# Kernel optimization log

Measured on AMD Instinct MI355X. Metric: run time of the kernel, lower is better.

## Reference

```python
import jax, jax.numpy as jnp
import numpy as np

B, N, D = 32, 2048, 320

def _init(key, shape, fan_in):
    return jax.random.normal(key, shape, dtype=jnp.float32) / np.sqrt(fan_in).astype(np.float32)

def setup_inputs() -> dict:
    key = jax.random.key(0)
    ks = jax.random.split(key, 11)
    return {
        "x": jax.random.normal(ks[0], (B, N, D), dtype=jnp.float32),
        # downs MLP: 320->160->80
        "W1": _init(ks[1], (320, 160), 320), "b1": jnp.zeros((160,), jnp.float32),
        "W2": _init(ks[2], (160, 80), 160),  "b2": jnp.zeros((80,), jnp.float32),
        # GraphConv1d layers: 80->40, 40->5
        "Wg1": _init(ks[3], (80, 40), 80),   "bg1": jnp.zeros((40,), jnp.float32),
        "Wg2": _init(ks[4], (40, 5), 40),    "bg2": jnp.zeros((5,), jnp.float32),
        # final classifier: 5->2
        "Wf": _init(ks[5], (5, 2), 5),       "bf": jnp.zeros((2,), jnp.float32),
    }

def _euclidean_adj(h):
    # h: [B, N, C] -> row-softmax of negative squared pairwise Euclidean distance [B, N, N]
    sq = jnp.sum(h * h, axis=-1, keepdims=True)               # [B, N, 1]
    d2 = sq - 2.0 * jnp.einsum('bnc,bmc->bnm', h, h) + jnp.swapaxes(sq, -1, -2)
    return jax.nn.softmax(-d2, axis=-1)

def _graph_conv(h, W, b):
    a = _euclidean_adj(h)                                     # dynamic adjacency
    agg = jnp.einsum('bnm,bmc->bnc', a, h)                    # neighbor aggregation
    return jax.nn.relu(agg @ W + b)

def reference(x, W1, b1, W2, b2, Wg1, bg1, Wg2, bg2, Wf, bf):
    h = jax.nn.relu(x @ W1 + b1)          # [B, N, 160]
    h = jax.nn.relu(h @ W2 + b2)          # [B, N, 80]
    h = _graph_conv(h, Wg1, bg1)          # [B, N, 40]
    h = _graph_conv(h, Wg2, bg2)          # [B, N, 5]
    h = jnp.mean(h, axis=1)               # Mean() over nodes -> [B, 5]
    logits = h @ Wf + bf                  # [B, 2]
    return jax.nn.softmax(logits, axis=-1)
```

## Files before the change

### kernel.cpp

```cpp
#include <hip/hip_runtime.h>
#include <math.h>

#define BB 32
#define NN 2048
#define D_IN 320
#define H1 160
#define H2 80
#define H4 5

typedef __attribute__((ext_vector_type(8))) short short8;
typedef __attribute__((ext_vector_type(4))) short short4v;
typedef __attribute__((ext_vector_type(4))) float f32x4;
typedef __attribute__((ext_vector_type(16))) float f32x16;

__device__ inline ushort f2bf(float f) {
    union { float f; unsigned u; } v; v.f = f;
    unsigned r = v.u + 0x7fff + ((v.u >> 16) & 1);
    return (ushort)(r >> 16);
}
__device__ inline float bf2f(ushort u) {
    union { float f; unsigned u; } v; v.u = ((unsigned)u) << 16;
    return v.f;
}
__device__ inline unsigned pkbf(float hi, float lo) {
    union { float f; unsigned u; } a, b; a.f = hi; b.f = lo;
    return __builtin_amdgcn_perm(a.u + 0x8000u, b.u + 0x8000u, 0x07060302u);
}
__device__ inline float fexp2(float x) {
    float r;
    asm("v_exp_f32 %0, %1" : "=v"(r) : "v"(x));
    return r;
}
union U2S { unsigned u[2]; short4v s; };
union U4S { unsigned u[4]; short8 s; short4v h[2]; };

#define LOG2E  1.44269504088896340736f
#define TWOL2E 2.88539008177792681472f

__global__ __launch_bounds__(256) void prep_weights_kernel(
    const float* __restrict__ W1, const float* __restrict__ W2,
    const float* __restrict__ Wg1, const float* __restrict__ bg1,
    const float* __restrict__ Wg2, const float* __restrict__ bg2,
    ushort* __restrict__ Wt1, ushort* __restrict__ Wt2,
    ushort* __restrict__ Wg1B, float* __restrict__ bg1P,
    ushort* __restrict__ Wg2A, float* __restrict__ bg2P)
{
    const int id0 = blockIdx.x * 256 + threadIdx.x;
    const int stride = gridDim.x * 256;
    for (int i = id0; i < H1 * D_IN; i += stride) {
        const int j = i / D_IN, c = i % D_IN;
        Wt1[i] = f2bf(W1[c * H1 + j]);
    }
    for (int i = id0; i < H2 * H1; i += stride) {
        const int j = i / H1, c = i % H1;
        Wt2[i] = f2bf(W2[c * H2 + j]);
    }
    for (int i = id0; i < 48 * 96; i += stride) {
        const int j = i / 96, c = i % 96;
        Wg1B[i] = (j < 40 && c < 80) ? f2bf(Wg1[c * 40 + j]) : (ushort)0;
    }
    for (int i = id0; i < 32 * 48; i += stride) {
        const int j = i / 48, c = i % 48;
        const int c4 = c & 15;
        const int pos = (c & ~15) + (c4 & 3) + (((c4 >> 3) & 1) << 2) + (((c4 >> 2) & 1) << 3);
        Wg2A[j * 48 + pos] = (j < 5 && c < 40) ? f2bf(Wg2[c * 5 + j]) : (ushort)0;
    }
    if (id0 < 64) bg1P[id0] = (id0 < 40) ? bg1[id0] : 0.f;
    if (id0 < 32) bg2P[id0] = (id0 < 5) ? bg2[id0] : 0.f;
}

__global__ __launch_bounds__(256) void mlp_mfma_kernel(
    const float* __restrict__ x,
    const ushort* __restrict__ Wt1, const float* __restrict__ b1,
    const ushort* __restrict__ Wt2, const float* __restrict__ b2,
    const ushort* __restrict__ Wg1B,
    ushort* __restrict__ h2, ushort* __restrict__ V1T, float* __restrict__ sq2)
{
    constexpr int XST  = 72;
    constexpr int W1ST = 72;
    constexpr int H1ST = 168;
    constexpr int RST  = 104;

    __shared__ __attribute__((aligned(16))) ushort h1t[64 * H1ST];
    __shared__ __attribute__((aligned(16))) ushort ws1[H1 * W1ST];
    __shared__ float b1s[H1];
    __shared__ float b2s[H2];

    ushort* xs = h1t;

    const int t = threadIdx.x;
    const int lane = t & 63, w = t >> 6;
    const int colid = lane & 15, quad = lane >> 4;
    const int i = blockIdx.x;
    const int b = ((i & 7) << 2) + ((i >> 3) & 3);
    const int n0 = (i >> 5) * 64;
    const int row0 = b * NN + n0;

    if (t < H1) b1s[t] = b1[t];
    if (t < H2) b2s[t] = b2[t];

    f32x4 c1[10];
    #pragma unroll
    for (int ns = 0; ns < 10; ++ns) c1[ns] = (f32x4){0.f, 0.f, 0.f, 0.f};

    float4 xr[4];
    short8 wr[5];
    {
        #pragma unroll
        for (int i2 = 0; i2 < 4; ++i2) {
            const int id = t + i2 * 256, row = id >> 4, c4 = id & 15;
            xr[i2] = *(const float4*)&x[(size_t)(row0 + row) * D_IN + c4 * 4];
        }
        #pragma unroll
        for (int i2 = 0; i2 < 5; ++i2) {
            const int id = t + i2 * 256, j = id >> 3, part = id & 7;
            wr[i2] = *(const short8*)&Wt1[j * D_IN + part * 8];
        }
    }

    for (int kc = 0; kc < 5; ++kc) {
        if (kc) __syncthreads();
        #pragma unroll
        for (int i2 = 0; i2 < 4; ++i2) {
            const int id = t + i2 * 256, row = id >> 4, c4 = id & 15;
            uint2 up;
            up.x = pkbf(xr[i2].y, xr[i2].x);
            up.y = pkbf(xr[i2].w, xr[i2].z);
            *(uint2*)&xs[row * XST + c4 * 4] = up;
        }
        #pragma unroll
        for (int i2 = 0; i2 < 5; ++i2) {
            const int id = t + i2 * 256, j = id >> 3, part = id & 7;
            *(short8*)&ws1[j * W1ST + part * 8] = wr[i2];
        }
        __syncthreads();
        if (kc < 4) {
            const int k0 = (kc + 1) * 64;
            #pragma unroll
            for (int i2 = 0; i2 < 4; ++i2) {
                const int id = t + i2 * 256, row = id >> 4, c4 = id & 15;
                xr[i2] = *(const float4*)&x[(size_t)(row0 + row) * D_IN + k0 + c4 * 4];
            }
            #pragma unroll
            for (int i2 = 0; i2 < 5; ++i2) {
                const int id = t + i2 * 256, j = id >> 3, part = id & 7;
                wr[i2] = *(const short8*)&Wt1[j * D_IN + k0 + part * 8];
            }
        }

        short8 af[2];
        #pragma unroll
        for (int kf = 0; kf < 2; ++kf)
            af[kf] = *(const short8*)&xs[(w * 16 + colid) * XST + kf * 32 + quad * 8];
        #pragma unroll
        for (int ns = 0; ns < 10; ++ns) {
            #pragma unroll
            for (int kf = 0; kf < 2; ++kf) {
                const short8 bf = *(const short8*)&ws1[(ns * 16 + colid) * W1ST + kf * 32 + quad * 8];
                c1[ns] = __builtin_amdgcn_mfma_f32_16x16x32_bf16(af[kf], bf, c1[ns], 0, 0, 0);
            }
        }
    }
    __syncthreads();

    #pragma unroll
    for (int ns = 0; ns < 10; ++ns) {
        const float bj = b1s[ns * 16 + colid];
        #pragma unroll
        for (int r = 0; r < 4; ++r)
            h1t[(w * 16 + quad * 4 + r) * H1ST + ns * 16 + colid] =
                f2bf(fmaxf(c1[ns][r] + bj, 0.f));
    }
    __asm__ volatile("s_waitcnt lgkmcnt(0)" ::: "memory");

    short8 a2[5];
    #pragma unroll
    for (int kf = 0; kf < 5; ++kf)
        a2[kf] = *(const short8*)&h1t[(w * 16 + colid) * H1ST + kf * 32 + quad * 8];

    f32x4 c2[5];
    #pragma unroll
    for (int js = 0; js < 5; ++js) {
        f32x4 acc = (f32x4){0.f, 0.f, 0.f, 0.f};
        #pragma unroll
        for (int kf = 0; kf < 5; ++kf) {
            const short8 wb = *(const short8*)&Wt2[(js * 16 + colid) * H1 + kf * 32 + quad * 8];
            acc = __builtin_amdgcn_mfma_f32_16x16x32_bf16(a2[kf], wb, acc, 0, 0, 0);
        }
        c2[js] = acc;
    }
    __syncthreads();

    ushort* h2row = h1t;
    float rsq[4] = {0.f, 0.f, 0.f, 0.f};
    #pragma unroll
    for (int js = 0; js < 5; ++js) {
        const float bj = b2s[js * 16 + colid];
        #pragma unroll
        for (int r = 0; r < 4; ++r) {
            const ushort u = f2bf(fmaxf(c2[js][r] + bj, 0.f));
            const float vv = bf2f(u);
            rsq[r] += vv * vv;
            h2[(size_t)(row0 + w * 16 + quad * 4 + r) * 80 + js * 16 + colid] = u;
            h2row[(w * 16 + quad * 4 + r) * RST + js * 16 + colid] = u;
        }
    }
    {
        const int zr = t >> 2, zc = t & 3;
        *(short4v*)&h2row[zr * RST + 80 + zc * 4] = (short4v){0, 0, 0, 0};
    }
    __asm__ volatile("s_waitcnt lgkmcnt(0)" ::: "memory");

    short8 a3[3];
    #pragma unroll
    for (int kf = 0; kf < 3; ++kf)
        a3[kf] = *(const short8*)&h2row[(w * 16 + colid) * RST + kf * 32 + quad * 8];

    f32x4 c3[3];
    #pragma unroll
    for (int js = 0; js < 3; ++js) {
        f32x4 acc = (f32x4){0.f, 0.f, 0.f, 0.f};
        #pragma unroll
        for (int kf = 0; kf < 3; ++kf) {
            const short8 wb = *(const short8*)&Wg1B[(js * 16 + colid) * 96 + kf * 32 + quad * 8];
            acc = __builtin_amdgcn_mfma_f32_16x16x32_bf16(a3[kf], wb, acc, 0, 0, 0);
        }
        c3[js] = acc;
    }

    #pragma unroll
    for (int m = 1; m <= 8; m <<= 1)
        #pragma unroll
        for (int r = 0; r < 4; ++r) rsq[r] += __shfl_xor(rsq[r], m);
    if (colid == 0) {
        #pragma unroll
        for (int r = 0; r < 4; ++r)
            sq2[(size_t)row0 + w * 16 + quad * 4 + r] = rsq[r] * 0.5f;
    }

    ushort* Tbuf = ws1;
    #pragma unroll
    for (int js = 0; js < 3; ++js)
        #pragma unroll
        for (int r = 0; r < 4; ++r)
            Tbuf[(js * 16 + colid) * 72 + w * 16 + quad * 4 + r] = f2bf(c3[js][r]);
    __syncthreads();
    const short8 ones8 = {16256, 16256, 16256, 16256, 16256, 16256, 16256, 16256};
    for (int id = t; id < 48 * 8; id += 256) {
        const int row = id >> 3, part = id & 7;
        const short8 val = (row == 40) ? ones8 : *(const short8*)&Tbuf[row * 72 + part * 8];
        *(short8*)&V1T[((size_t)b * 48 + row) * NN + n0 + part * 8] = val;
    }
}

template<int CK, int CV, int CVS, int ONES_CH, bool HAS_OUT, bool DO_MEAN, int C_OUT>
__global__ __launch_bounds__(512, 2) void attn_conv_kernel(
    const ushort* __restrict__ h, const ushort* __restrict__ hT,
    const float* __restrict__ sqg,
    const ushort* __restrict__ WtP, const float* __restrict__ biasP,
    ushort* __restrict__ ho, ushort* __restrict__ hoT, float* __restrict__ sqo,
    float* __restrict__ mean_out)
{
    constexpr int CF   = CK / 16;
    constexpr int CSV  = CV / 32;
    constexpr int KST  = CK + 8;
    constexpr int VST  = 64 + 8;
    constexpr int KPR  = CK / 8;
    constexpr int KTOT = 64 * KPR;
    constexpr int NK   = (KTOT + 255) / 256;
    constexpr int VTOT = CVS * 8;
    constexpr int NV   = (VTOT + 255) / 256;
    constexpr int TST  = 136;
    constexpr int CS1  = ONES_CH / 32;
    constexpr int R1v  = ((ONES_CH % 32) / 8) * 4 + (ONES_CH & 3);
    constexpr int BUFN = 64 * KST + CVS * VST;
    constexpr int NITH = NN / 128;
    constexpr int ESTR = CSV * 16 + 4;

    __shared__ __attribute__((aligned(16))) ushort ldsbuf[2][2][BUFN];
    __shared__ __attribute__((aligned(16))) float sqs[2][2][64];

    const int t = threadIdx.x;
    const int lane = t & 63, w = t >> 6;
    const int qw = w & 3, kh = w >> 2;
    const int th = t & 255;
    const int m32 = lane & 31, hl = lane >> 5;
    const int i = blockIdx.x;
    const int b = ((i & 7) << 2) + ((i >> 3) & 3);
    const int n0blk = (i >> 5) * 128;
    const int qrow = n0blk + qw * 32 + m32;
    const int kbase = kh * (NN / 2);

    short8 qf[CF];
    {
        const ushort* qr = h + ((size_t)b * NN + qrow) * CK;
        #pragma unroll
        for (int c = 0; c < CF; ++c)
            qf[c] = *(const short8*)&qr[c * 16 + hl * 8];
    }
    const float nsqn = -sqg[(size_t)b * NN + qrow];

    f32x16 o[CSV];
    #pragma unroll
    for (int cs = 0; cs < CSV; ++cs)
        #pragma unroll
        for (int r = 0; r < 16; ++r) o[cs][r] = 0.f;

    short8 kreg[NK], vreg[NV];
    float sqreg = 0.f;

    auto loadTile = [&](int n1) {
        const ushort* hsrc = h + ((size_t)b * NN + n1) * CK;
        #pragma unroll
        for (int i2 = 0; i2 < NK; ++i2) {
            const int id = th + i2 * 256;
            if (KTOT % 256 == 0 || id < KTOT)
                kreg[i2] = *(const short8*)&hsrc[id * 8];
        }
        #pragma unroll
        for (int i2 = 0; i2 < NV; ++i2) {
            const int id = th + i2 * 256;
            if (VTOT % 256 == 0 || id < VTOT) {
                const int c = id >> 3, pt = id & 7;
                vreg[i2] = *(const short8*)&hT[((size_t)b * CVS + c) * NN + n1 + pt * 8];
            }
        }
        if (th < 64) sqreg = sqg[(size_t)b * NN + n1 + th];
    };
    auto stageTile = [&](int buf) {
        ushort* Kd = ldsbuf[kh][buf];
        ushort* Vd = Kd + 64 * KST;
        #pragma unroll
        for (int i2 = 0; i2 < NK; ++i2) {
            const int id = th + i2 * 256;
            if (KTOT % 256 == 0 || id < KTOT) {
                const int row = id / KPR, pt = id % KPR;
                *(short8*)&Kd[row * KST + pt * 8] = kreg[i2];
            }
        }
        #pragma unroll
        for (int i2 = 0; i2 < NV; ++i2) {
            const int id = th + i2 * 256;
            if (VTOT % 256 == 0 || id < VTOT) {
                const int c = id >> 3, pt = id & 7;
                const int colb = ((pt >> 1) << 4) + ((pt & 1) << 2);
                U4S vv; vv.s = vreg[i2];
                *(short4v*)&Vd[c * VST + colb]     = vv.h[0];
                *(short4v*)&Vd[c * VST + colb + 8] = vv.h[1];
            }
        }
        if (th < 64) sqs[kh][buf][th] = sqreg;
    };

    auto preloadK = [&](const ushort* Krow, short8 (&kf)[2][CF]) {
        #pragma unroll
        for (int T = 0; T < 2; ++T)
            #pragma unroll
            for (int c = 0; c < CF; ++c)
                kf[T][c] = *(const short8*)&Krow[(T * 32 + m32) * KST + c * 16 + hl * 8];
    };
    auto initST = [&](int buf, f32x16& s0, f32x16& s1) {
        #pragma unroll
        for (int g = 0; g < 4; ++g) {
            const f32x4 sm0 = *(const f32x4*)&sqs[kh][buf][g * 8 + hl * 4];
            const f32x4 sm1 = *(const f32x4*)&sqs[kh][buf][32 + g * 8 + hl * 4];
            #pragma unroll
            for (int r2 = 0; r2 < 4; ++r2) {
                s0[g * 4 + r2] = nsqn - sm0[r2];
                s1[g * 4 + r2] = nsqn - sm1[r2];
            }
        }
    };
    auto smfma = [&](short8 (&kf)[2][CF], f32x16& s0, f32x16& s1) {
        #pragma unroll
        for (int c = 0; c < CF; ++c) {
            s0 = __builtin_amdgcn_mfma_f32_32x32x16_bf16(kf[0][c], qf[c], s0, 0, 0, 0);
            s1 = __builtin_amdgcn_mfma_f32_32x32x16_bf16(kf[1][c], qf[c], s1, 0, 0, 0);
        }
    };
    auto readV = [&](const ushort* Vcol, short8 (&vf)[2][2][CSV]) {
        const short8 z8 = {0, 0, 0, 0, 0, 0, 0, 0};
        #pragma unroll
        for (int T = 0; T < 2; ++T)
            #pragma unroll
            for (int c = 0; c < 2; ++c)
                #pragma unroll
                for (int cs = 0; cs < CSV; ++cs) {
                    const int row = cs * 32 + m32;
                    vf[T][c][cs] = (row < CVS)
                        ? *(const short8*)&Vcol[row * VST + (T * 2 + c) * 16 + hl * 8]
                        : z8;
                }
    };
    auto expPV = [&](const f32x16& s0, const f32x16& s1, const short8 (&vf)[2][2][CSV]) {
        #pragma unroll
        for (int T = 0; T < 2; ++T) {
            const f32x16& st = T ? s1 : s0;
            float p[16];
            #pragma unroll
            for (int g = 0; g < 4; ++g)
                #pragma unroll
                for (int r2 = 0; r2 < 4; ++r2)
                    p[g * 4 + r2] = fexp2(st[g * 4 + r2] * TWOL2E);
            #pragma unroll
            for (int c = 0; c < 2; ++c) {
                U4S pk_;
                #pragma unroll
                for (int bq = 0; bq < 4; ++bq)
                    pk_.u[bq] = pkbf(p[c * 8 + bq * 2 + 1], p[c * 8 + bq * 2]);
                #pragma unroll
                for (int cs = 0; cs < CSV; ++cs)
                    o[cs] = __builtin_amdgcn_mfma_f32_32x32x16_bf16(vf[T][c][cs], pk_.s, o[cs], 0, 0, 0);
            }
        }
    };

    loadTile(kbase);
    stageTile(0);
    __syncthreads();
    loadTile(kbase + 64);

    #pragma unroll 1
    for (int it = 0; it < NITH; ++it) {
        const int cur = it & 1;
        const ushort* Krow = ldsbuf[kh][cur];
        const ushort* Vcol = Krow + 64 * KST;

        short8 kf[2][CF];
        f32x16 s0, s1;
        preloadK(Krow, kf);
        initST(cur, s0, s1);

        if (it + 1 < NITH) stageTile(cur ^ 1);
        if (it + 2 < NITH) loadTile(kbase + (it + 2) * 64);

        smfma(kf, s0, s1);
        short8 vf[2][2][CSV];
        readV(Vcol, vf);
        expPV(s0, s1, vf);
        __syncthreads();
    }

    float* exch = (float*)&ldsbuf[0][0][0];
    if (kh == 1) {
        #pragma unroll
        for (int cs = 0; cs < CSV; ++cs)
            #pragma unroll
            for (int g = 0; g < 4; ++g) {
                f32x4 v;
                #pragma unroll
                for (int j = 0; j < 4; ++j) v[j] = o[cs][g * 4 + j];
                *(f32x4*)&exch[(qw * 64 + lane) * ESTR + cs * 16 + g * 4] = v;
            }
    }
    __syncthreads();
    if (kh == 0) {
        #pragma unroll
        for (int cs = 0; cs < CSV; ++cs)
            #pragma unroll
            for (int g = 0; g < 4; ++g) {
                const f32x4 v = *(const f32x4*)&exch[(qw * 64 + lane) * ESTR + cs * 16 + g * 4];
                #pragma unroll
                for (int j = 0; j < 4; ++j) o[cs][g * 4 + j] += v[j];
            }
    }

    float rsv = (hl == 0) ? o[CS1][R1v] : 0.f;
    rsv += __shfl_xor(rsv, 32);
    const float rinv = 1.f / rsv;

    if constexpr (DO_MEAN) {
        if (kh == 0) {
            float msum[4];
            #pragma unroll
            for (int r2 = 0; r2 < 4; ++r2)
                msum[r2] = fmaxf(o[0][r2] * rinv + biasP[hl * 4 + r2], 0.f);
            #pragma unroll
            for (int s = 1; s <= 16; s <<= 1)
                #pragma unroll
                for (int r2 = 0; r2 < 4; ++r2) msum[r2] += __shfl_xor(msum[r2], s);
            if (m32 == 0) {
                if (hl == 0) {
                    #pragma unroll
                    for (int r2 = 0; r2 < 4; ++r2)
                        atomicAdd(&mean_out[b * C_OUT + r2], msum[r2] * (1.f / NN));
                } else {
                    atomicAdd(&mean_out[b * C_OUT + 4], msum[0] * (1.f / NN));
                }
            }
        }
    }

    if constexpr (HAS_OUT) {
        __syncthreads();
        ushort* Tbuf = (ushort*)&ldsbuf[0][0][0];
        if (kh == 0) {
            float vv[CSV][16];
            float rsq = 0.f;
            #pragma unroll
            for (int cs = 0; cs < CSV; ++cs) {
                #pragma unroll
                for (int g = 0; g < 4; ++g) {
                    const int jb = cs * 32 + g * 8 + hl * 4;
                    const f32x4 bv = *(const f32x4*)&biasP[jb];
                    float v[4];
                    #pragma unroll
                    for (int r2 = 0; r2 < 4; ++r2) {
                        float val = fmaxf(o[cs][g * 4 + r2] * rinv + bv[r2], 0.f);
                        if (cs == CS1 && g * 4 + r2 == R1v) val = 0.f;
                        v[r2] = val;
                        vv[cs][g * 4 + r2] = val;
                    }
                    if (jb < 48) {
                        U2S uo;
                        uo.u[0] = pkbf(v[1], v[0]);
                        uo.u[1] = pkbf(v[3], v[2]);
                        *(short4v*)&ho[((size_t)b * NN + qrow) * 48 + jb] = uo.s;
                        #pragma unroll
                        for (int r2 = 0; r2 < 4; ++r2) {
                            const float vs = bf2f((ushort)(uo.u[r2 >> 1] >> ((r2 & 1) * 16)));
                            rsq += vs * vs;
                        }
                    }
                }
            }
            const float rsq2 = rsq + __shfl_xor(rsq, 32);
            if (hl == 0) sqo[(size_t)b * NN + qrow] = rsq2 * 0.5f;

            short8 ob2[3];
            #pragma unroll
            for (int cc = 0; cc < 3; ++cc) {
                const int cs = cc >> 1, c2 = cc & 1;
                U4S ob_;
                #pragma unroll
                for (int bq = 0; bq < 4; ++bq)
                    ob_.u[bq] = pkbf(vv[cs][c2 * 8 + bq * 2 + 1], vv[cs][c2 * 8 + bq * 2]);
                ob2[cc] = ob_.s;
            }
            f32x16 acc;
            #pragma unroll
            for (int r = 0; r < 16; ++r) acc[r] = 0.f;
            #pragma unroll
            for (int cc = 0; cc < 3; ++cc) {
                const short8 wa = *(const short8*)&WtP[(size_t)m32 * 48 + cc * 16 + hl * 8];
                acc = __builtin_amdgcn_mfma_f32_32x32x16_bf16(wa, ob2[cc], acc, 0, 0, 0);
            }

            #pragma unroll
            for (int g = 0; g < 2; ++g)
                #pragma unroll
                for (int r2 = 0; r2 < 4; ++r2)
                    Tbuf[(g * 8 + hl * 4 + r2) * TST + qw * 32 + m32] = f2bf(acc[g * 4 + r2]);
        }
        __syncthreads();
        const short8 ones8 = {16256, 16256, 16256, 16256, 16256, 16256, 16256, 16256};
        if (t < 256) {
            const int row = t >> 4, part = t & 15;
            const short8 val = (row == 8) ? ones8
                             : *(const short8*)&Tbuf[row * TST + part * 8];
            *(short8*)&hoT[((size_t)b * 16 + row) * NN + n0blk + part * 8] = val;
        }
    }
}

__global__ __launch_bounds__(64) void final_kernel(
    const float* __restrict__ mean, const float* __restrict__ Wf,
    const float* __restrict__ bf, float* __restrict__ out)
{
    const int t = threadIdx.x;
    const int b = t >> 1, k = t & 1;
    float acc = bf[k];
    #pragma unroll
    for (int c = 0; c < H4; ++c) acc += mean[b * H4 + c] * Wf[c * 2 + k];
    const float other = __shfl_xor(acc, 1);
    const float mx = fmaxf(acc, other);
    const float e  = __expf(acc - mx);
    const float eo = __expf(other - mx);
    out[t] = e / (e + eo);
}

extern "C" void kernel_launch(void* const* d_in, const int* in_sizes, int n_in,
                              void* d_out, int out_size, void* d_ws, size_t ws_size,
                              hipStream_t stream) {
    const float* x   = (const float*)d_in[0];
    const float* W1  = (const float*)d_in[1];
    const float* b1  = (const float*)d_in[2];
    const float* W2  = (const float*)d_in[3];
    const float* b2  = (const float*)d_in[4];
    const float* Wg1 = (const float*)d_in[5];
    const float* bg1 = (const float*)d_in[6];
    const float* Wg2 = (const float*)d_in[7];
    const float* bg2 = (const float*)d_in[8];
    const float* Wf  = (const float*)d_in[9];
    const float* bf  = (const float*)d_in[10];

    ushort* h2   = (ushort*)d_ws;
    ushort* V1T  = h2  + (size_t)BB * NN * 80;
    float*  sq2  = (float*)(V1T + (size_t)BB * 48 * NN);
    ushort* h3   = (ushort*)(sq2 + (size_t)BB * NN);
    ushort* V2T  = h3  + (size_t)BB * NN * 48;
    float*  sq3  = (float*)(V2T + (size_t)BB * 16 * NN);
    float*  meanb = sq3 + (size_t)BB * NN;
    ushort* Wt1  = (ushort*)(meanb + 160);
    ushort* Wt2  = Wt1 + (size_t)H1 * D_IN;
    ushort* Wg1B = Wt2 + (size_t)H2 * H1;
    float*  bg1P = (float*)(Wg1B + 48 * 96);
    ushort* Wg2A = (ushort*)(bg1P + 64);
    float*  bg2P = (float*)(Wg2A + 32 * 48);

    hipMemsetAsync(meanb, 0, BB * H4 * sizeof(float), stream);

    prep_weights_kernel<<<64, 256, 0, stream>>>(W1, W2, Wg1, bg1, Wg2, bg2,
                                                Wt1, Wt2, Wg1B, bg1P, Wg2A, bg2P);
    mlp_mfma_kernel<<<BB * NN / 64, 256, 0, stream>>>(x, Wt1, b1, Wt2, b2, Wg1B,
                                                      h2, V1T, sq2);
    attn_conv_kernel<80, 64, 48, 40, true,  false, 0><<<BB * NN / 128, 512, 0, stream>>>(
        h2, V1T, sq2, Wg2A, bg1P, h3, V2T, sq3, nullptr);
    attn_conv_kernel<48, 32, 16, 8,  false, true,  5><<<BB * NN / 128, 512, 0, stream>>>(
        h3, V2T, sq3, nullptr, bg2P, nullptr, nullptr, nullptr, meanb);
    final_kernel<<<1, 64, 0, stream>>>(meanb, Wf, bf, (float*)d_out);
}
```

Before: 273.0 us.

## Split attention-conv into separate key-split partial and combine kernels

The fused 512-thread attention kernel, which split keys across two wave halves and reduced them through LDS, is replaced by a 256-thread partial kernel launched per key-split block, plus a combine kernel. The partial kernel writes fp32 partial accumulators to global memory, and the combine kernel sums them and applies the normalization, bias, ReLU, next-layer projection and mean epilogue. The aim is finer-grained blocks for better scheduling and occupancy, and a shorter epilogue. The cost is extra launches and a global round trip for the partial outputs.

```diff
diff --git a/kernel.cpp b/kernel.cpp
--- a/kernel.cpp
+++ b/kernel.cpp
@@ -253,13 +253,10 @@
     }
 }
 
-template<int CK, int CV, int CVS, int ONES_CH, bool HAS_OUT, bool DO_MEAN, int C_OUT>
-__global__ __launch_bounds__(512, 2) void attn_conv_kernel(
+template<int CK, int CV, int CVS, int KSPLIT>
+__global__ __launch_bounds__(256, 2) void attn_part_kernel(
     const ushort* __restrict__ h, const ushort* __restrict__ hT,
-    const float* __restrict__ sqg,
-    const ushort* __restrict__ WtP, const float* __restrict__ biasP,
-    ushort* __restrict__ ho, ushort* __restrict__ hoT, float* __restrict__ sqo,
-    float* __restrict__ mean_out)
+    const float* __restrict__ sqg, float* __restrict__ pO)
 {
     constexpr int CF   = CK / 16;
     constexpr int CSV  = CV / 32;
@@ -270,26 +267,22 @@
     constexpr int NK   = (KTOT + 255) / 256;
     constexpr int VTOT = CVS * 8;
     constexpr int NV   = (VTOT + 255) / 256;
-    constexpr int TST  = 136;
-    constexpr int CS1  = ONES_CH / 32;
-    constexpr int R1v  = ((ONES_CH % 32) / 8) * 4 + (ONES_CH & 3);
     constexpr int BUFN = 64 * KST + CVS * VST;
-    constexpr int NITH = NN / 128;
-    constexpr int ESTR = CSV * 16 + 4;
-
-    __shared__ __attribute__((aligned(16))) ushort ldsbuf[2][2][BUFN];
-    __shared__ __attribute__((aligned(16))) float sqs[2][2][64];
+    constexpr int NITH = NN / 64 / KSPLIT;
+
+    __shared__ __attribute__((aligned(16))) ushort ldsbuf[2][BUFN];
+    __shared__ __attribute__((aligned(16))) float sqs[2][64];
 
     const int t = threadIdx.x;
     const int lane = t & 63, w = t >> 6;
-    const int qw = w & 3, kh = w >> 2;
-    const int th = t & 255;
     const int m32 = lane & 31, hl = lane >> 5;
-    const int i = blockIdx.x;
-    const int b = ((i & 7) << 2) + ((i >> 3) & 3);
-    const int n0blk = (i >> 5) * 128;
-    const int qrow = n0blk + qw * 32 + m32;
-    const int kbase = kh * (NN / 2);
+    const int gi = blockIdx.x;
+    const int ks = gi & (KSPLIT - 1);
+    const int qblk = gi / KSPLIT;
+    const int b = ((qblk & 7) << 2) + ((qblk >> 3) & 3);
+    const int n0blk = (qblk >> 5) * 128;
+    const int qrow = n0blk + w * 32 + m32;
+    const int kbase = ks * (NN / KSPLIT);
 
     short8 qf[CF];
     {
@@ -313,26 +306,26 @@
         const ushort* hsrc = h + ((size_t)b * NN + n1) * CK;
         #pragma unroll
         for (int i2 = 0; i2 < NK; ++i2) {
-            const int id = th + i2 * 256;
+            const int id = t + i2 * 256;
             if (KTOT % 256 == 0 || id < KTOT)
                 kreg[i2] = *(const short8*)&hsrc[id * 8];
         }
         #pragma unroll
         for (int i2 = 0; i2 < NV; ++i2) {
-            const int id = th + i2 * 256;
+            const int id = t + i2 * 256;
             if (VTOT % 256 == 0 || id < VTOT) {
                 const int c = id >> 3, pt = id & 7;
                 vreg[i2] = *(const short8*)&hT[((size_t)b * CVS + c) * NN + n1 + pt * 8];
             }
         }
-        if (th < 64) sqreg = sqg[(size_t)b * NN + n1 + th];
+        if (t < 64) sqreg = sqg[(size_t)b * NN + n1 + t];
     };
     auto stageTile = [&](int buf) {
-        ushort* Kd = ldsbuf[kh][buf];
+        ushort* Kd = ldsbuf[buf];
         ushort* Vd = Kd + 64 * KST;
         #pragma unroll
         for (int i2 = 0; i2 < NK; ++i2) {
-            const int id = th + i2 * 256;
+            const int id = t + i2 * 256;
             if (KTOT % 256 == 0 || id < KTOT) {
                 const int row = id / KPR, pt = id % KPR;
                 *(short8*)&Kd[row * KST + pt * 8] = kreg[i2];
@@ -340,7 +333,7 @@
         }
         #pragma unroll
         for (int i2 = 0; i2 < NV; ++i2) {
-            const int id = th + i2 * 256;
+            const int id = t + i2 * 256;
             if (VTOT % 256 == 0 || id < VTOT) {
                 const int c = id >> 3, pt = id & 7;
                 const int colb = ((pt >> 1) << 4) + ((pt & 1) << 2);
@@ -349,7 +342,7 @@
                 *(short4v*)&Vd[c * VST + colb + 8] = vv.h[1];
             }
         }
-        if (th < 64) sqs[kh][buf][th] = sqreg;
+        if (t < 64) sqs[buf][t] = sqreg;
     };
 
     auto preloadK = [&](const ushort* Krow, short8 (&kf)[2][CF]) {
@@ -362,8 +355,8 @@
     auto initST = [&](int buf, f32x16& s0, f32x16& s1) {
         #pragma unroll
         for (int g = 0; g < 4; ++g) {
-            const f32x4 sm0 = *(const f32x4*)&sqs[kh][buf][g * 8 + hl * 4];
-            const f32x4 sm1 = *(const f32x4*)&sqs[kh][buf][32 + g * 8 + hl * 4];
+            const f32x4 sm0 = *(const f32x4*)&sqs[buf][g * 8 + hl * 4];
+            const f32x4 sm1 = *(const f32x4*)&sqs[buf][32 + g * 8 + hl * 4];
             #pragma unroll
             for (int r2 = 0; r2 < 4; ++r2) {
                 s0[g * 4 + r2] = nsqn - sm0[r2];
@@ -423,7 +416,7 @@
     #pragma unroll 1
     for (int it = 0; it < NITH; ++it) {
         const int cur = it & 1;
-        const ushort* Krow = ldsbuf[kh][cur];
+        const ushort* Krow = ldsbuf[cur];
         const ushort* Vcol = Krow + 64 * KST;
 
         short8 kf[2][CF];
@@ -441,120 +434,132 @@
         __syncthreads();
     }
 
-    float* exch = (float*)&ldsbuf[0][0][0];
-    if (kh == 1) {
+    #pragma unroll
+    for (int cs = 0; cs < CSV; ++cs)
+        #pragma unroll
+        for (int r = 0; r < 16; ++r)
+            pO[((((size_t)qblk * KSPLIT + ks) * CSV + cs) * 16 + r) * 256 + t] = o[cs][r];
+}
+
+template<int CV, int CVS, int ONES_CH, bool HAS_OUT, bool DO_MEAN, int C_OUT, int KSPLIT>
+__global__ __launch_bounds__(256) void attn_combine_kernel(
+    const float* __restrict__ pO,
+    const ushort* __restrict__ WtP, const float* __restrict__ biasP,
+    ushort* __restrict__ ho, ushort* __restrict__ hoT, float* __restrict__ sqo,
+    float* __restrict__ mean_out)
+{
+    constexpr int CSV = CV / 32;
+    constexpr int TST = 136;
+    constexpr int CS1 = ONES_CH / 32;
+    constexpr int R1v = ((ONES_CH % 32) / 8) * 4 + (ONES_CH & 3);
+
+    __shared__ __attribute__((aligned(16))) ushort Tbuf[16 * TST];
+
+    const int t = threadIdx.x;
+    const int lane = t & 63, w = t >> 6;
+    const int m32 = lane & 31, hl = lane >> 5;
+    const int i = blockIdx.x;
+    const int b = ((i & 7) << 2) + ((i >> 3) & 3);
+    const int n0blk = (i >> 5) * 128;
+    const int qrow = n0blk + w * 32 + m32;
+
+    f32x16 o[CSV];
+    #pragma unroll
+    for (int cs = 0; cs < CSV; ++cs)
+        #pragma unroll
+        for (int r = 0; r < 16; ++r) o[cs][r] = 0.f;
+    #pragma unroll
+    for (int ks = 0; ks < KSPLIT; ++ks)
         #pragma unroll
         for (int cs = 0; cs < CSV; ++cs)
             #pragma unroll
-            for (int g = 0; g < 4; ++g) {
-                f32x4 v;
-                #pragma unroll
-                for (int j = 0; j < 4; ++j) v[j] = o[cs][g * 4 + j];
-                *(f32x4*)&exch[(qw * 64 + lane) * ESTR + cs * 16 + g * 4] = v;
-            }
-    }
-    __syncthreads();
-    if (kh == 0) {
-        #pragma unroll
-        for (int cs = 0; cs < CSV; ++cs)
-            #pragma unroll
-            for (int g = 0; g < 4; ++g) {
-                const f32x4 v = *(const f32x4*)&exch[(qw * 64 + lane) * ESTR + cs * 16 + g * 4];
-                #pragma unroll
-                for (int j = 0; j < 4; ++j) o[cs][g * 4 + j] += v[j];
-            }
-    }
+            for (int r = 0; r < 16; ++r)
+                o[cs][r] += pO[((((size_t)i * KSPLIT + ks) * CSV + cs) * 16 + r) * 256 + t];
 
     float rsv = (hl == 0) ? o[CS1][R1v] : 0.f;
     rsv += __shfl_xor(rsv, 32);
     const float rinv = 1.f / rsv;
 
     if constexpr (DO_MEAN) {
-        if (kh == 0) {
-            float msum[4];
-            #pragma unroll
-            for (int r2 = 0; r2 < 4; ++r2)
-                msum[r2] = fmaxf(o[0][r2] * rinv + biasP[hl * 4 + r2], 0.f);
-            #pragma unroll
-            for (int s = 1; s <= 16; s <<= 1)
+        float msum[4];
+        #pragma unroll
+        for (int r2 = 0; r2 < 4; ++r2)
+            msum[r2] = fmaxf(o[0][r2] * rinv + biasP[hl * 4 + r2], 0.f);
+        #pragma unroll
+        for (int s = 1; s <= 16; s <<= 1)
+            #pragma unroll
+            for (int r2 = 0; r2 < 4; ++r2) msum[r2] += __shfl_xor(msum[r2], s);
+        if (m32 == 0) {
+            if (hl == 0) {
                 #pragma unroll
-                for (int r2 = 0; r2 < 4; ++r2) msum[r2] += __shfl_xor(msum[r2], s);
-            if (m32 == 0) {
-                if (hl == 0) {
-                    #pragma unroll
-                    for (int r2 = 0; r2 < 4; ++r2)
-                        atomicAdd(&mean_out[b * C_OUT + r2], msum[r2] * (1.f / NN));
-                } else {
-                    atomicAdd(&mean_out[b * C_OUT + 4], msum[0] * (1.f / NN));
+                for (int r2 = 0; r2 < 4; ++r2)
+                    atomicAdd(&mean_out[b * C_OUT + r2], msum[r2] * (1.f / NN));
+            } else {
+                atomicAdd(&mean_out[b * C_OUT + 4], msum[0] * (1.f / NN));
+            }
+        }
+    }
+
+    if constexpr (HAS_OUT) {
+        float vv[CSV][16];
+        float rsq = 0.f;
+        #pragma unroll
+        for (int cs = 0; cs < CSV; ++cs) {
+            #pragma unroll
+            for (int g = 0; g < 4; ++g) {
+                const int jb = cs * 32 + g * 8 + hl * 4;
+                const f32x4 bv = *(const f32x4*)&biasP[jb];
+                float v[4];
+                #pragma unroll
+                for (int r2 = 0; r2 < 4; ++r2) {
+                    float val = fmaxf(o[cs][g * 4 + r2] * rinv + bv[r2], 0.f);
+                    if (cs == CS1 && g * 4 + r2 == R1v) val = 0.f;
+                    v[r2] = val;
+                    vv[cs][g * 4 + r2] = val;
                 }
-            }
-        }
-    }
-
-    if constexpr (HAS_OUT) {
-        __syncthreads();
-        ushort* Tbuf = (ushort*)&ldsbuf[0][0][0];
-        if (kh == 0) {
-            float vv[CSV][16];
-            float rsq = 0.f;
-            #pragma unroll
-            for (int cs = 0; cs < CSV; ++cs) {
-                #pragma unroll
-                for (int g = 0; g < 4; ++g) {
-                    const int jb = cs * 32 + g * 8 + hl * 4;
-                    const f32x4 bv = *(const f32x4*)&biasP[jb];
-                    float v[4];
+                if (jb < 48) {
+                    U2S uo;
+                    uo.u[0] = pkbf(v[1], v[0]);
+                    uo.u[1] = pkbf(v[3], v[2]);
+                    *(short4v*)&ho[((size_t)b * NN + qrow) * 48 + jb] = uo.s;
                     #pragma unroll
                     for (int r2 = 0; r2 < 4; ++r2) {
-                        float val = fmaxf(o[cs][g * 4 + r2] * rinv + bv[r2], 0.f);
-                        if (cs == CS1 && g * 4 + r2 == R1v) val = 0.f;
-                        v[r2] = val;
-                        vv[cs][g * 4 + r2] = val;
-                    }
-                    if (jb < 48) {
-                        U2S uo;
-                        uo.u[0] = pkbf(v[1], v[0]);
-                        uo.u[1] = pkbf(v[3], v[2]);
-                        *(short4v*)&ho[((size_t)b * NN + qrow) * 48 + jb] = uo.s;
-                        #pragma unroll
-                        for (int r2 = 0; r2 < 4; ++r2) {
-                            const float vs = bf2f((ushort)(uo.u[r2 >> 1] >> ((r2 & 1) * 16)));
-                            rsq += vs * vs;
-                        }
+                        const float vs = bf2f((ushort)(uo.u[r2 >> 1] >> ((r2 & 1) * 16)));
+                        rsq += vs * vs;
                     }
                 }
             }
-            const float rsq2 = rsq + __shfl_xor(rsq, 32);
-            if (hl == 0) sqo[(size_t)b * NN + qrow] = rsq2 * 0.5f;
-
-            short8 ob2[3];
-            #pragma unroll
-            for (int cc = 0; cc < 3; ++cc) {
-                const int cs = cc >> 1, c2 = cc & 1;
-                U4S ob_;
-                #pragma unroll
-                for (int bq = 0; bq < 4; ++bq)
-                    ob_.u[bq] = pkbf(vv[cs][c2 * 8 + bq * 2 + 1], vv[cs][c2 * 8 + bq * 2]);
-                ob2[cc] = ob_.s;
-            }
-            f32x16 acc;
-            #pragma unroll
-            for (int r = 0; r < 16; ++r) acc[r] = 0.f;
-            #pragma unroll
-            for (int cc = 0; cc < 3; ++cc) {
-                const short8 wa = *(const short8*)&WtP[(size_t)m32 * 48 + cc * 16 + hl * 8];
-                acc = __builtin_amdgcn_mfma_f32_32x32x16_bf16(wa, ob2[cc], acc, 0, 0, 0);
-            }
-
-            #pragma unroll
-            for (int g = 0; g < 2; ++g)
-                #pragma unroll
-                for (int r2 = 0; r2 < 4; ++r2)
-                    Tbuf[(g * 8 + hl * 4 + r2) * TST + qw * 32 + m32] = f2bf(acc[g * 4 + r2]);
-        }
+        }
+        const float rsq2 = rsq + __shfl_xor(rsq, 32);
+        if (hl == 0) sqo[(size_t)b * NN + qrow] = rsq2 * 0.5f;
+
+        short8 ob2[3];
+        #pragma unroll
+        for (int cc = 0; cc < 3; ++cc) {
+            const int cs = cc >> 1, c2 = cc & 1;
+            U4S ob_;
+            #pragma unroll
+            for (int bq = 0; bq < 4; ++bq)
+                ob_.u[bq] = pkbf(vv[cs][c2 * 8 + bq * 2 + 1], vv[cs][c2 * 8 + bq * 2]);
+            ob2[cc] = ob_.s;
+        }
+        f32x16 acc;
+        #pragma unroll
+        for (int r = 0; r < 16; ++r) acc[r] = 0.f;
+        #pragma unroll
+        for (int cc = 0; cc < 3; ++cc) {
+            const short8 wa = *(const short8*)&WtP[(size_t)m32 * 48 + cc * 16 + hl * 8];
+            acc = __builtin_amdgcn_mfma_f32_32x32x16_bf16(wa, ob2[cc], acc, 0, 0, 0);
+        }
+
+        #pragma unroll
+        for (int g = 0; g < 2; ++g)
+            #pragma unroll
+            for (int r2 = 0; r2 < 4; ++r2)
+                Tbuf[(g * 8 + hl * 4 + r2) * TST + w * 32 + m32] = f2bf(acc[g * 4 + r2]);
         __syncthreads();
         const short8 ones8 = {16256, 16256, 16256, 16256, 16256, 16256, 16256, 16256};
-        if (t < 256) {
+        {
             const int row = t >> 4, part = t & 15;
             const short8 val = (row == 8) ? ones8
                              : *(const short8*)&Tbuf[row * TST + part * 8];
@@ -607,6 +612,7 @@
     float*  bg1P = (float*)(Wg1B + 48 * 96);
     ushort* Wg2A = (ushort*)(bg1P + 64);
     float*  bg2P = (float*)(Wg2A + 32 * 48);
+    float*  pO   = bg2P + 32;
 
     hipMemsetAsync(meanb, 0, BB * H4 * sizeof(float), stream);
 
@@ -614,9 +620,13 @@
                                                 Wt1, Wt2, Wg1B, bg1P, Wg2A, bg2P);
     mlp_mfma_kernel<<<BB * NN / 64, 256, 0, stream>>>(x, Wt1, b1, Wt2, b2, Wg1B,
                                                       h2, V1T, sq2);
-    attn_conv_kernel<80, 64, 48, 40, true,  false, 0><<<BB * NN / 128, 512, 0, stream>>>(
-        h2, V1T, sq2, Wg2A, bg1P, h3, V2T, sq3, nullptr);
-    attn_conv_kernel<48, 32, 16, 8,  false, true,  5><<<BB * NN / 128, 512, 0, stream>>>(
-        h3, V2T, sq3, nullptr, bg2P, nullptr, nullptr, nullptr, meanb);
+    attn_part_kernel<80, 64, 48, 2><<<BB * NN / 128 * 2, 256, 0, stream>>>(
+        h2, V1T, sq2, pO);
+    attn_combine_kernel<64, 48, 40, true, false, 0, 2><<<BB * NN / 128, 256, 0, stream>>>(
+        pO, Wg2A, bg1P, h3, V2T, sq3, nullptr);
+    attn_part_kernel<48, 32, 16, 2><<<BB * NN / 128 * 2, 256, 0, stream>>>(
+        h3, V2T, sq3, pO);
+    attn_combine_kernel<32, 16, 8, false, true, 5, 2><<<BB * NN / 128, 256, 0, stream>>>(
+        pO, nullptr, bg2P, nullptr, nullptr, nullptr, meanb);
     final_kernel<<<1, 64, 0, stream>>>(meanb, Wf, bf, (float*)d_out);
 }
```

Result: slower. 290.6 us (+6.4%).
